# Kernel optimization log

Hardware: AMD Instinct MI355X
Metric: run time of the kernel (lower is better)

## Reference

```python
import jax, jax.numpy as jnp
import numpy as np

R = 32            # voxel resolution
DIM = 240         # channels C
EPS_NORM = 0.0    # module eps
BN_EPS = 1e-5     # torch BatchNorm1d default eps


def setup_inputs() -> dict:
    key = jax.random.key(0)
    k1, k2, k3 = jax.random.split(key, 3)
    B, C, N = 4, DIM, 32768
    features = jax.random.normal(k1, (B, C, N), jnp.float32)
    coords = jax.random.uniform(k2, (B, 3, N), jnp.float32)
    # mlp params: Conv1d(2C -> C, kernel 1) + BatchNorm1d(C)
    w = jax.random.normal(k3, (C, 2 * C), jnp.float32) / np.sqrt(2 * C).astype(np.float32)
    b = jnp.zeros((C,), jnp.float32)
    gamma = jnp.ones((C,), jnp.float32)
    beta = jnp.zeros((C,), jnp.float32)
    return {"features": features, "coords": coords, "w": w, "b": b, "gamma": gamma, "beta": beta}


def _voxelize(features, coords):
    # normalize coords into [0, 1], scale to voxel grid
    nc = coords - coords.mean(axis=2, keepdims=True)                      # [B,3,N]
    scale = jnp.linalg.norm(nc, axis=1, keepdims=True).max(axis=2, keepdims=True) * 2.0 + EPS_NORM
    nc = nc / scale + 0.5
    nc = jnp.clip(nc * R, 0, R - 1)
    vox = jnp.round(nc).astype(jnp.int32)
    pos = vox[:, 0] + vox[:, 1] * R + vox[:, 2] * (R * R)                 # [B,N] flattened voxel id
    R3 = R * R * R

    def per_batch(f, p):
        # f: [C,N], p: [N] -> [2C, R3]; per-voxel max feature + second (min) feature
        mx = jax.ops.segment_max(f.T, p, num_segments=R3)                 # [R3, C]
        mn = jax.ops.segment_min(f.T, p, num_segments=R3)                 # [R3, C]
        cnt = jax.ops.segment_sum(jnp.ones_like(p), p, num_segments=R3)  # [R3]
        mask = (cnt > 0)[:, None]
        mx = jnp.where(mask, mx, 0.0)
        mn = jnp.where(mask, mn, 0.0)
        return jnp.concatenate([mx, mn], axis=1).T                        # [2C, R3]

    fea = jax.vmap(per_batch)(features, pos)                              # [B,2C,R3]
    return fea, nc


def reference(features, coords, w, b, gamma, beta):
    fea, nc = _voxelize(features, coords)
    # 1x1 Conv1d (pointwise GEMM) + BatchNorm1d (training-mode batch stats) + Swish
    y = jnp.einsum('co,bov->bcv', w, fea) + b[None, :, None]
    mean = y.mean(axis=(0, 2), keepdims=True)
    var = y.var(axis=(0, 2), keepdims=True)
    y = gamma[None, :, None] * (y - mean) * jax.lax.rsqrt(var + BN_EPS) + beta[None, :, None]
    y = y * jax.nn.sigmoid(y)
    B, C, _ = features.shape
    return y.reshape(B, C, R, R, R), nc
```

## Files before the change

kernel.cpp:

```cpp
#include <hip/hip_runtime.h>
#include <cstdint>
#include <cstddef>

#define RR 32
#define R3 32768
#define NPT 32768
#define CH 240
#define CH2 480
#define NB 4
#define Y_ELEMS 31457280

typedef __attribute__((ext_vector_type(8))) short short8v;
typedef __attribute__((ext_vector_type(4))) float float4v;

union u8pack { short8v v; unsigned short u[8]; };

static __device__ __forceinline__ float bf2f(unsigned short u) {
  return __uint_as_float(((unsigned int)u) << 16);
}
static __device__ __forceinline__ unsigned short f2bf(float f) {
  unsigned int u = __float_as_uint(f);
  u = (u + 0x7FFFu + ((u >> 16) & 1u)) >> 16;
  return (unsigned short)u;
}

static __device__ __forceinline__ void gl_lds16(const void* g, void* l) {
  __builtin_amdgcn_global_load_lds((const __attribute__((address_space(1))) unsigned int*)g,
                                   (__attribute__((address_space(3))) unsigned int*)l, 16, 0, 0);
}

__global__ void k_init(int* __restrict__ cnt, float* __restrict__ stats,
                       const float* __restrict__ w, unsigned short* __restrict__ wfrag) {
  int g = blockIdx.x * 256 + threadIdx.x;
  if (g < NB * R3) cnt[g] = 0;
  if (g < 1024) stats[g] = 0.0f;
  if (g < 14400) {
    int lane = g & 63, t = g >> 6;
    int mg = t / 75, r = t % 75;
    int kc = r / 5, mL = r % 5;
    int m = mg * 5 + mL;
    int ln = lane & 15, q = lane >> 4;
    const float* src = w + (size_t)(m * 16 + ln) * CH2 + kc * 32 + q * 8;
    u8pack pk;
#pragma unroll
    for (int j = 0; j < 8; j++) pk.u[j] = f2bf(src[j]);
    *(short8v*)&wfrag[(size_t)g * 8] = pk.v;
  }
}

__global__ __launch_bounds__(1024) void k_coord_stats(const float* __restrict__ coords,
                                                      float* __restrict__ ms) {
  __shared__ float red[1024];
  __shared__ float mean[3];
  int b = blockIdx.x, t = threadIdx.x;
  const float4* cb4 = (const float4*)(coords + (size_t)b * 3 * NPT);
  float s[3] = {0.f, 0.f, 0.f};
  for (int i = t; i < NPT / 4; i += 1024) {
#pragma unroll
    for (int d = 0; d < 3; d++) {
      float4 v = cb4[d * (NPT / 4) + i];
      s[d] += (v.x + v.y) + (v.z + v.w);
    }
  }
  for (int d = 0; d < 3; d++) {
    red[t] = s[d]; __syncthreads();
    for (int k = 512; k > 0; k >>= 1) { if (t < k) red[t] += red[t + k]; __syncthreads(); }
    if (t == 0) mean[d] = red[0] * (1.0f / NPT);
    __syncthreads();
  }
  float m0 = mean[0], m1 = mean[1], m2 = mean[2];
  float mx = 0.f;
  for (int i = t; i < NPT / 4; i += 1024) {
    float4 x = cb4[i], y = cb4[NPT / 4 + i], z = cb4[2 * (NPT / 4) + i];
    float dx, dy, dz, n;
    dx = x.x - m0; dy = y.x - m1; dz = z.x - m2; n = dx * dx + dy * dy + dz * dz; mx = fmaxf(mx, n);
    dx = x.y - m0; dy = y.y - m1; dz = z.y - m2; n = dx * dx + dy * dy + dz * dz; mx = fmaxf(mx, n);
    dx = x.z - m0; dy = y.z - m1; dz = z.z - m2; n = dx * dx + dy * dy + dz * dz; mx = fmaxf(mx, n);
    dx = x.w - m0; dy = y.w - m1; dz = z.w - m2; n = dx * dx + dy * dy + dz * dz; mx = fmaxf(mx, n);
  }
  red[t] = mx; __syncthreads();
  for (int k = 512; k > 0; k >>= 1) { if (t < k) red[t] = fmaxf(red[t], red[t + k]); __syncthreads(); }
  if (t == 0) {
    ms[b * 4 + 0] = m0; ms[b * 4 + 1] = m1; ms[b * 4 + 2] = m2;
    ms[b * 4 + 3] = sqrtf(red[0]) * 2.0f;
  }
}

__global__ void k_pos_nc(const float* __restrict__ coords, const float* __restrict__ ms,
                         float* __restrict__ ncout, int* __restrict__ pos, int* __restrict__ cnt) {
  int g = blockIdx.x * 256 + threadIdx.x;
  int b = g >> 15, i = g & (NPT - 1);
  const float* cb = coords + (size_t)b * 3 * NPT;
  float scale = ms[b * 4 + 3];
  int vox[3];
#pragma unroll
  for (int d = 0; d < 3; d++) {
    float v = (cb[(size_t)d * NPT + i] - ms[b * 4 + d]) / scale + 0.5f;
    v = fminf(fmaxf(v * (float)RR, 0.0f), (float)(RR - 1));
    ncout[((size_t)(b * 3 + d)) * NPT + i] = v;
    vox[d] = (int)rintf(v);
  }
  int p = (b << 15) | (vox[0] + (vox[1] << 5) + (vox[2] << 10));
  pos[g] = p;
  atomicAdd(&cnt[p], 1);
}

__global__ void k_scan(const int* __restrict__ cnt, int* __restrict__ offs) {
  __shared__ int part[1024];
  int b = blockIdx.x, t = threadIdx.x;
  const int base = b * R3;
  int local[32];
  int s = 0;
#pragma unroll
  for (int j = 0; j < 32; j++) { local[j] = cnt[base + t * 32 + j]; s += local[j]; }
  part[t] = s; __syncthreads();
  for (int d = 1; d < 1024; d <<= 1) {
    int v = (t >= d) ? part[t - d] : 0;
    __syncthreads();
    part[t] += v;
    __syncthreads();
  }
  int run = (t == 0) ? 0 : part[t - 1];
#pragma unroll
  for (int j = 0; j < 32; j++) { offs[base + t * 32 + j] = run; run += local[j]; }
}

__global__ void k_scatter(const int* __restrict__ pos, int* __restrict__ offs,
                          int* __restrict__ sorted) {
  int g = blockIdx.x * 256 + threadIdx.x;
  int p = pos[g];
  int slot = atomicAdd(&offs[p], 1);
  sorted[((g >> 15) << 15) + slot] = g;
}

__global__ void k_transpose3(const float* __restrict__ f, unsigned short* __restrict__ ft) {
  __shared__ float tile[CH * 65];
  int p0 = blockIdx.x * 64, b = blockIdx.y;
  int t = threadIdx.x;
  {
    int pp = t & 63, cq = t >> 6;
    const float* src = f + ((size_t)b * CH) * NPT + p0 + pp;
#pragma unroll 4
    for (int j = 0; j < 60; ++j) {
      int c = j * 4 + cq;
      tile[c * 65 + pp] = src[(size_t)c * NPT];
    }
  }
  __syncthreads();
  int ch8 = t & 7;
#pragma unroll
  for (int pass = 0; pass < 2; ++pass) {
    int p = pass * 32 + (t >> 3);
    unsigned short* dst = ft + ((size_t)(b * NPT + p0 + p)) * CH;
#pragma unroll
    for (int i = 0; i < 4; ++i) {
      int ch = ch8 + 8 * i;
      if (ch < 30) {
        u8pack pk;
#pragma unroll
        for (int jj = 0; jj < 8; ++jj) pk.u[jj] = f2bf(tile[(ch * 8 + jj) * 65 + p]);
        *(short8v*)&dst[ch * 8] = pk.v;
      }
    }
  }
}

__global__ __launch_bounds__(256) void k_voxel4(const int* __restrict__ cnt,
                                                const int* __restrict__ offs,
                                                const int* __restrict__ sorted,
                                                const unsigned short* __restrict__ ft,
                                                unsigned short* __restrict__ feaf) {
  __shared__ unsigned short sh[7680];
  int bcg = blockIdx.x;
  int b = bcg >> 11;
  int wave = threadIdx.x >> 6, lane = threadIdx.x & 63;
  int sub = lane >> 5, l = lane & 31;
  int vbase = bcg << 4;
#pragma unroll
  for (int it = 0; it < 2; ++it) {
    int ln = wave + 8 * it + 4 * sub;
    if (l < 30) {
      int v = vbase + ln;
      int t0 = l, t1 = 30 + l;
      int idx0 = (t0 >> 2) * 512 + ((t0 & 3) * 16 + ln) * 8;
      int idx1 = (t1 >> 2) * 512 + ((t1 & 3) * 16 + ln) * 8;
      int n = cnt[v];
      if (n == 0) {
        u8pack z;
#pragma unroll
        for (int j = 0; j < 8; j++) z.u[j] = 0;
        *(short8v*)&sh[idx0] = z.v;
        *(short8v*)&sh[idx1] = z.v;
      } else {
        int start = offs[v] - n;
        const int* sp = sorted + (b << 15) + start;
        float mx[8], mn[8];
#pragma unroll
        for (int j = 0; j < 8; j++) { mx[j] = -__builtin_inff(); mn[j] = __builtin_inff(); }
        int j = 0;
        for (; j + 2 <= n; j += 2) {
          int r0 = sp[j], r1 = sp[j + 1];
          u8pack u0, u1;
          u0.v = *(const short8v*)(ft + (size_t)r0 * CH + l * 8);
          u1.v = *(const short8v*)(ft + (size_t)r1 * CH + l * 8);
#pragma unroll
          for (int k = 0; k < 8; k++) {
            float a = bf2f(u0.u[k]), c = bf2f(u1.u[k]);
            mx[k] = fmaxf(mx[k], fmaxf(a, c));
            mn[k] = fminf(mn[k], fminf(a, c));
          }
        }
        if (j < n) {
          int r0 = sp[j];
          u8pack u0;
          u0.v = *(const short8v*)(ft + (size_t)r0 * CH + l * 8);
#pragma unroll
          for (int k = 0; k < 8; k++) {
            float a = bf2f(u0.u[k]);
            mx[k] = fmaxf(mx[k], a);
            mn[k] = fminf(mn[k], a);
          }
        }
        u8pack omx, omn;
#pragma unroll
        for (int k = 0; k < 8; k++) { omx.u[k] = f2bf(mx[k]); omn.u[k] = f2bf(mn[k]); }
        *(short8v*)&sh[idx0] = omx.v;
        *(short8v*)&sh[idx1] = omn.v;
      }
    }
  }
  __syncthreads();
  unsigned short* dst = feaf + (size_t)bcg * 7680;
  for (int i = threadIdx.x; i < 960; i += 256)
    *(int4*)&dst[i * 8] = *(const int4*)&sh[i * 8];
}

__global__ __launch_bounds__(256, 2) void k_gemm6(const unsigned short* __restrict__ wfrag,
                                                  const unsigned short* __restrict__ feaf,
                                                  const float* __restrict__ bias,
                                                  unsigned short* __restrict__ ybf,
                                                  float* __restrict__ gstats) {
  __shared__ unsigned short wl[75 * 512];
  __shared__ float bstats[160];
  int wave = threadIdx.x >> 6, lane = threadIdx.x & 63;
  int ln = lane & 15, q = lane >> 4;
  int mg = blockIdx.y, bz = blockIdx.z;

  for (int i = threadIdx.x; i < 160; i += 256) bstats[i] = 0.0f;

  {
    const unsigned short* gs = wfrag + (size_t)mg * 75 * 512 + lane * 8;
    for (int i = wave; i < 75; i += 4) gl_lds16(gs + i * 512, wl + i * 512);
  }

  int v0 = blockIdx.x * 256 + wave * 64;
  int cg0 = v0 >> 4;
  const unsigned short* fbb = feaf + ((size_t)(bz * 2048 + cg0) * 15) * 512 + lane * 8;

  float4v acc[5][4];
#pragma unroll
  for (int m = 0; m < 5; m++)
#pragma unroll
    for (int j = 0; j < 4; j++) acc[m][j] = (float4v){0.f, 0.f, 0.f, 0.f};

  short8v cb0 = *(const short8v*)(fbb + (size_t)(0 * 15 + 0) * 512);
  short8v cb1 = *(const short8v*)(fbb + (size_t)(1 * 15 + 0) * 512);
  short8v cb2 = *(const short8v*)(fbb + (size_t)(2 * 15 + 0) * 512);
  short8v cb3 = *(const short8v*)(fbb + (size_t)(3 * 15 + 0) * 512);

  __syncthreads();

#pragma unroll
  for (int kc = 0; kc < 15; ++kc) {
    short8v nb0, nb1, nb2, nb3;
    if (kc < 14) {
      nb0 = *(const short8v*)(fbb + (size_t)(0 * 15 + kc + 1) * 512);
      nb1 = *(const short8v*)(fbb + (size_t)(1 * 15 + kc + 1) * 512);
      nb2 = *(const short8v*)(fbb + (size_t)(2 * 15 + kc + 1) * 512);
      nb3 = *(const short8v*)(fbb + (size_t)(3 * 15 + kc + 1) * 512);
    }
    const unsigned short* wp = wl + (size_t)(kc * 5) * 512 + lane * 8;
#pragma unroll
    for (int mL = 0; mL < 5; ++mL) {
      short8v a = *(const short8v*)(wp + (size_t)mL * 512);
      acc[mL][0] = __builtin_amdgcn_mfma_f32_16x16x32_bf16(a, cb0, acc[mL][0], 0, 0, 0);
      acc[mL][1] = __builtin_amdgcn_mfma_f32_16x16x32_bf16(a, cb1, acc[mL][1], 0, 0, 0);
      acc[mL][2] = __builtin_amdgcn_mfma_f32_16x16x32_bf16(a, cb2, acc[mL][2], 0, 0, 0);
      acc[mL][3] = __builtin_amdgcn_mfma_f32_16x16x32_bf16(a, cb3, acc[mL][3], 0, 0, 0);
    }
    if (kc < 14) { cb0 = nb0; cb1 = nb1; cb2 = nb2; cb3 = nb3; }
  }

  unsigned short* yb = ybf + ((size_t)bz * CH) * R3 + v0 + ln;
#pragma unroll
  for (int mL = 0; mL < 5; ++mL) {
#pragma unroll
    for (int r = 0; r < 4; ++r) {
      int cl = mL * 16 + q * 4 + r;
      int c = mg * 80 + cl;
      float bb = bias[c];
      float y0 = acc[mL][0][r] + bb;
      float y1 = acc[mL][1][r] + bb;
      float y2 = acc[mL][2][r] + bb;
      float y3 = acc[mL][3][r] + bb;
      unsigned short* yrow = yb + (size_t)c * R3;
      yrow[0] = f2bf(y0); yrow[16] = f2bf(y1); yrow[32] = f2bf(y2); yrow[48] = f2bf(y3);
      float s = (y0 + y1) + (y2 + y3);
      float sq = (y0 * y0 + y1 * y1) + (y2 * y2 + y3 * y3);
#pragma unroll
      for (int off = 1; off < 16; off <<= 1) {
        s += __shfl_xor(s, off);
        sq += __shfl_xor(sq, off);
      }
      if (ln == 0) {
        atomicAdd(&bstats[cl], s);
        atomicAdd(&bstats[80 + cl], sq);
      }
    }
  }
  __syncthreads();
  for (int i = threadIdx.x; i < 160; i += 256) {
    int g = (i < 80) ? (mg * 80 + i) : (CH + mg * 80 + (i - 80));
    atomicAdd(&gstats[g], bstats[i]);
  }
}

__global__ void k_apply(const unsigned short* __restrict__ ybf, float* __restrict__ out,
                        const float* __restrict__ stats, const float* __restrict__ gamma,
                        const float* __restrict__ beta) {
  int g = blockIdx.x * 256 + threadIdx.x;
  int c = (g >> 12) % CH;
  const float ninv = 1.0f / (float)(NB * R3);
  float mean = stats[c] * ninv;
  float var = stats[CH + c] * ninv - mean * mean;
  float s = gamma[c] * rsqrtf(var + 1e-5f);
  float h = beta[c] - mean * s;
  u8pack v;
  v.v = *(const short8v*)(ybf + (size_t)g * 8);
  float4 o0, o1;
  float t;
  t = bf2f(v.u[0]) * s + h; o0.x = t / (1.0f + __expf(-t));
  t = bf2f(v.u[1]) * s + h; o0.y = t / (1.0f + __expf(-t));
  t = bf2f(v.u[2]) * s + h; o0.z = t / (1.0f + __expf(-t));
  t = bf2f(v.u[3]) * s + h; o0.w = t / (1.0f + __expf(-t));
  t = bf2f(v.u[4]) * s + h; o1.x = t / (1.0f + __expf(-t));
  t = bf2f(v.u[5]) * s + h; o1.y = t / (1.0f + __expf(-t));
  t = bf2f(v.u[6]) * s + h; o1.z = t / (1.0f + __expf(-t));
  t = bf2f(v.u[7]) * s + h; o1.w = t / (1.0f + __expf(-t));
  ((float4*)out)[(size_t)g * 2] = o0;
  ((float4*)out)[(size_t)g * 2 + 1] = o1;
}

extern "C" void kernel_launch(void* const* d_in, const int* in_sizes, int n_in,
                              void* d_out, int out_size, void* d_ws, size_t ws_size,
                              hipStream_t stream) {
  const float* features = (const float*)d_in[0];
  const float* coords   = (const float*)d_in[1];
  const float* w        = (const float*)d_in[2];
  const float* bias     = (const float*)d_in[3];
  const float* gamma    = (const float*)d_in[4];
  const float* beta     = (const float*)d_in[5];
  float* out = (float*)d_out;

  char* ws = (char*)d_ws;
  size_t off = 0;
  float* ms    = (float*)(ws + off); off += 256;
  float* stats = (float*)(ws + off); off += 4096;
  int* pos     = (int*)(ws + off);   off += (size_t)NB * NPT * 4;
  int* cnt     = (int*)(ws + off);   off += (size_t)NB * R3 * 4;
  int* offs    = (int*)(ws + off);   off += (size_t)NB * R3 * 4;
  int* sorted  = (int*)(ws + off);   off += (size_t)NB * NPT * 4;
  unsigned short* wfrag = (unsigned short*)(ws + off); off += (size_t)CH * CH2 * 2;
  unsigned short* ft    = (unsigned short*)(ws + off); off += (size_t)NB * NPT * CH * 2;
  unsigned short* feaf  = (unsigned short*)(ws + off); off += (size_t)NB * R3 * CH2 * 2;
  unsigned short* ybf   = ft;

  float* ncout = out + Y_ELEMS;

  k_init<<<516, 256, 0, stream>>>(cnt, stats, w, wfrag);
  k_coord_stats<<<4, 1024, 0, stream>>>(coords, ms);
  k_pos_nc<<<512, 256, 0, stream>>>(coords, ms, ncout, pos, cnt);
  k_scan<<<4, 1024, 0, stream>>>(cnt, offs);
  k_scatter<<<512, 256, 0, stream>>>(pos, offs, sorted);
  k_transpose3<<<dim3(512, 4), 256, 0, stream>>>(features, ft);
  k_voxel4<<<NB * 2048, 256, 0, stream>>>(cnt, offs, sorted, ft, feaf);
  k_gemm6<<<dim3(128, 3, NB), 256, 0, stream>>>(wfrag, feaf, bias, ybf, stats);
  k_apply<<<Y_ELEMS / 2048, 256, 0, stream>>>(ybf, out, stats, gamma, beta);
}
```

Before: 399.0 us.

## Fuse voxel reduction into GEMM and write transposed features in sorted order

The transpose kernel now scatters each point's bf16 feature row straight to its voxel-sorted slot, using a per-point rank from the scatter kernel. The voxel max/min gather therefore reads contiguous rows and no longer chases indices. The voxel reduction is fused with the 1x1-conv GEMM in one 512-thread kernel: pooled features stay in swizzled LDS, and each wave keeps its weight fragments in registers across all 240 output channels. This drops the feaf intermediate round-trip through global memory and a kernel launch. The cost is higher register and LDS pressure, plus scattered writes in the transpose.

```diff
diff --git a/kernel.cpp b/kernel.cpp
--- a/kernel.cpp
+++ b/kernel.cpp
@@ -22,11 +22,6 @@
   unsigned int u = __float_as_uint(f);
   u = (u + 0x7FFFu + ((u >> 16) & 1u)) >> 16;
   return (unsigned short)u;
-}
-
-static __device__ __forceinline__ void gl_lds16(const void* g, void* l) {
-  __builtin_amdgcn_global_load_lds((const __attribute__((address_space(1))) unsigned int*)g,
-                                   (__attribute__((address_space(3))) unsigned int*)l, 16, 0, 0);
 }
 
 __global__ void k_init(int* __restrict__ cnt, float* __restrict__ stats,
@@ -126,17 +121,20 @@
 }
 
 __global__ void k_scatter(const int* __restrict__ pos, int* __restrict__ offs,
-                          int* __restrict__ sorted) {
+                          int* __restrict__ rank) {
   int g = blockIdx.x * 256 + threadIdx.x;
   int p = pos[g];
   int slot = atomicAdd(&offs[p], 1);
-  sorted[((g >> 15) << 15) + slot] = g;
-}
-
-__global__ void k_transpose3(const float* __restrict__ f, unsigned short* __restrict__ ft) {
+  rank[g] = slot;
+}
+
+__global__ void k_transpose3(const float* __restrict__ f, const int* __restrict__ rank,
+                             unsigned short* __restrict__ fts) {
   __shared__ float tile[CH * 65];
+  __shared__ int slts[64];
   int p0 = blockIdx.x * 64, b = blockIdx.y;
   int t = threadIdx.x;
+  if (t < 64) slts[t] = rank[b * NPT + p0 + t];
   {
     int pp = t & 63, cq = t >> 6;
     const float* src = f + ((size_t)b * CH) * NPT + p0 + pp;
@@ -151,7 +149,7 @@
 #pragma unroll
   for (int pass = 0; pass < 2; ++pass) {
     int p = pass * 32 + (t >> 3);
-    unsigned short* dst = ft + ((size_t)(b * NPT + p0 + p)) * CH;
+    unsigned short* dst = fts + ((size_t)(b * NPT + slts[p])) * CH;
 #pragma unroll
     for (int i = 0; i < 4; ++i) {
       int ch = ch8 + 8 * i;
@@ -165,55 +163,70 @@
   }
 }
 
-__global__ __launch_bounds__(256) void k_voxel4(const int* __restrict__ cnt,
-                                                const int* __restrict__ offs,
-                                                const int* __restrict__ sorted,
-                                                const unsigned short* __restrict__ ft,
-                                                unsigned short* __restrict__ feaf) {
-  __shared__ unsigned short sh[7680];
-  int bcg = blockIdx.x;
-  int b = bcg >> 11;
-  int wave = threadIdx.x >> 6, lane = threadIdx.x & 63;
+__global__ __launch_bounds__(512, 2) void k_fused(const int* __restrict__ cnt,
+                                                  const int* __restrict__ offs,
+                                                  const unsigned short* __restrict__ fts,
+                                                  const unsigned short* __restrict__ wfrag,
+                                                  const float* __restrict__ bias,
+                                                  unsigned short* __restrict__ ybf,
+                                                  float* __restrict__ gstats) {
+  __shared__ unsigned short fB[8 * 15 * 512];
+  __shared__ float bstats[480];
+  int tid = threadIdx.x;
+  int wave = tid >> 6, lane = tid & 63;
   int sub = lane >> 5, l = lane & 31;
-  int vbase = bcg << 4;
-#pragma unroll
-  for (int it = 0; it < 2; ++it) {
-    int ln = wave + 8 * it + 4 * sub;
+  int ln = lane & 15, q = lane >> 4;
+  int b = blockIdx.y;
+  int v0 = blockIdx.x * 128;
+  int bbase = b << 15;
+
+  for (int i = tid; i < 480; i += 512) bstats[i] = 0.0f;
+
+  int proc = wave * 2 + sub;
+  int t1c = 30 + l;
+  int kc0 = l >> 2, q0 = l & 3;
+  int kc1 = t1c >> 2, q1 = t1c & 3;
+#pragma unroll 1
+  for (int it = 0; it < 8; ++it) {
     if (l < 30) {
-      int v = vbase + ln;
-      int t0 = l, t1 = 30 + l;
-      int idx0 = (t0 >> 2) * 512 + ((t0 & 3) * 16 + ln) * 8;
-      int idx1 = (t1 >> 2) * 512 + ((t1 & 3) * 16 + ln) * 8;
+      int v = bbase + v0 + it * 16 + proc;
+      int ci0 = (q0 * 16 + proc) ^ ((kc0 & 3) << 1);
+      int ci1 = (q1 * 16 + proc) ^ ((kc1 & 3) << 1);
+      int idx0 = ((it * 15 + kc0) * 64 + ci0) * 8;
+      int idx1 = ((it * 15 + kc1) * 64 + ci1) * 8;
       int n = cnt[v];
       if (n == 0) {
         u8pack z;
 #pragma unroll
-        for (int j = 0; j < 8; j++) z.u[j] = 0;
-        *(short8v*)&sh[idx0] = z.v;
-        *(short8v*)&sh[idx1] = z.v;
+        for (int k = 0; k < 8; k++) z.u[k] = 0;
+        *(short8v*)&fB[idx0] = z.v;
+        *(short8v*)&fB[idx1] = z.v;
       } else {
         int start = offs[v] - n;
-        const int* sp = sorted + (b << 15) + start;
+        const unsigned short* sp = fts + (size_t)(bbase + start) * CH + l * 8;
         float mx[8], mn[8];
 #pragma unroll
-        for (int j = 0; j < 8; j++) { mx[j] = -__builtin_inff(); mn[j] = __builtin_inff(); }
+        for (int k = 0; k < 8; k++) { mx[k] = -__builtin_inff(); mn[k] = __builtin_inff(); }
         int j = 0;
-        for (; j + 2 <= n; j += 2) {
-          int r0 = sp[j], r1 = sp[j + 1];
-          u8pack u0, u1;
-          u0.v = *(const short8v*)(ft + (size_t)r0 * CH + l * 8);
-          u1.v = *(const short8v*)(ft + (size_t)r1 * CH + l * 8);
+        for (; j + 4 <= n; j += 4) {
+          u8pack u0, u1, u2, u3;
+          u0.v = *(const short8v*)(sp);
+          u1.v = *(const short8v*)(sp + CH);
+          u2.v = *(const short8v*)(sp + 2 * CH);
+          u3.v = *(const short8v*)(sp + 3 * CH);
+          sp += 4 * CH;
 #pragma unroll
           for (int k = 0; k < 8; k++) {
-            float a = bf2f(u0.u[k]), c = bf2f(u1.u[k]);
-            mx[k] = fmaxf(mx[k], fmaxf(a, c));
-            mn[k] = fminf(mn[k], fminf(a, c));
+            float a0 = bf2f(u0.u[k]), a1 = bf2f(u1.u[k]);
+            float a2 = bf2f(u2.u[k]), a3 = bf2f(u3.u[k]);
+            mx[k] = fmaxf(mx[k], fmaxf(fmaxf(a0, a1), fmaxf(a2, a3)));
+            mn[k] = fminf(mn[k], fminf(fminf(a0, a1), fminf(a2, a3)));
           }
         }
-        if (j < n) {
-          int r0 = sp[j];
+        for (; j < n; ++j) {
           u8pack u0;
-          u0.v = *(const short8v*)(ft + (size_t)r0 * CH + l * 8);
+          u0.v = *(const short8v*)(sp);
+          sp += CH;
 #pragma unroll
           for (int k = 0; k < 8; k++) {
             float a = bf2f(u0.u[k]);
@@ -224,103 +237,79 @@
         u8pack omx, omn;
 #pragma unroll
         for (int k = 0; k < 8; k++) { omx.u[k] = f2bf(mx[k]); omn.u[k] = f2bf(mn[k]); }
-        *(short8v*)&sh[idx0] = omx.v;
-        *(short8v*)&sh[idx1] = omn.v;
+        *(short8v*)&fB[idx0] = omx.v;
+        *(short8v*)&fB[idx1] = omn.v;
       }
     }
   }
+
+  int nmt = (wave == 7) ? 1 : 2;
+  short8v wreg[2][15];
+#pragma unroll
+  for (int mm = 0; mm < 2; ++mm)
+    if (mm < nmt) {
+      int mt = wave * 2 + mm;
+      int mg = mt / 5, mL = mt % 5;
+      const unsigned short* wp = wfrag + ((size_t)(mg * 75 + mL) * 512) + lane * 8;
+#pragma unroll
+      for (int kc = 0; kc < 15; ++kc)
+        wreg[mm][kc] = *(const short8v*)(wp + (size_t)kc * 5 * 512);
+    }
+
   __syncthreads();
-  unsigned short* dst = feaf + (size_t)bcg * 7680;
-  for (int i = threadIdx.x; i < 960; i += 256)
-    *(int4*)&dst[i * 8] = *(const int4*)&sh[i * 8];
-}
-
-__global__ __launch_bounds__(256, 2) void k_gemm6(const unsigned short* __restrict__ wfrag,
-                                                  const unsigned short* __restrict__ feaf,
-                                                  const float* __restrict__ bias,
-                                                  unsigned short* __restrict__ ybf,
-                                                  float* __restrict__ gstats) {
-  __shared__ unsigned short wl[75 * 512];
-  __shared__ float bstats[160];
-  int wave = threadIdx.x >> 6, lane = threadIdx.x & 63;
-  int ln = lane & 15, q = lane >> 4;
-  int mg = blockIdx.y, bz = blockIdx.z;
-
-  for (int i = threadIdx.x; i < 160; i += 256) bstats[i] = 0.0f;
-
-  {
-    const unsigned short* gs = wfrag + (size_t)mg * 75 * 512 + lane * 8;
-    for (int i = wave; i < 75; i += 4) gl_lds16(gs + i * 512, wl + i * 512);
-  }
-
-  int v0 = blockIdx.x * 256 + wave * 64;
-  int cg0 = v0 >> 4;
-  const unsigned short* fbb = feaf + ((size_t)(bz * 2048 + cg0) * 15) * 512 + lane * 8;
-
-  float4v acc[5][4];
-#pragma unroll
-  for (int m = 0; m < 5; m++)
-#pragma unroll
-    for (int j = 0; j < 4; j++) acc[m][j] = (float4v){0.f, 0.f, 0.f, 0.f};
-
-  short8v cb0 = *(const short8v*)(fbb + (size_t)(0 * 15 + 0) * 512);
-  short8v cb1 = *(const short8v*)(fbb + (size_t)(1 * 15 + 0) * 512);
-  short8v cb2 = *(const short8v*)(fbb + (size_t)(2 * 15 + 0) * 512);
-  short8v cb3 = *(const short8v*)(fbb + (size_t)(3 * 15 + 0) * 512);
-
+
+  float4v acc[2][8];
+#pragma unroll
+  for (int mm = 0; mm < 2; ++mm)
+#pragma unroll
+    for (int cg = 0; cg < 8; ++cg) acc[mm][cg] = (float4v){0.f, 0.f, 0.f, 0.f};
+
+#pragma unroll
+  for (int kc = 0; kc < 15; ++kc) {
+    const unsigned short* fbl = fB + (size_t)((lane ^ ((kc & 3) << 1)) * 8);
+    short8v bf[8];
+#pragma unroll
+    for (int cg = 0; cg < 8; ++cg)
+      bf[cg] = *(const short8v*)(fbl + (size_t)(cg * 15 + kc) * 512);
+#pragma unroll
+    for (int mm = 0; mm < 2; ++mm)
+      if (mm < nmt)
+#pragma unroll
+        for (int cg = 0; cg < 8; ++cg)
+          acc[mm][cg] = __builtin_amdgcn_mfma_f32_16x16x32_bf16(wreg[mm][kc], bf[cg], acc[mm][cg], 0, 0, 0);
+  }
+
+  unsigned short* yb = ybf + ((size_t)b * CH) * R3 + v0 + ln;
+#pragma unroll
+  for (int mm = 0; mm < 2; ++mm)
+    if (mm < nmt) {
+      int mt = wave * 2 + mm;
+#pragma unroll
+      for (int r = 0; r < 4; ++r) {
+        int c = mt * 16 + q * 4 + r;
+        float bb = bias[c];
+        unsigned short* yrow = yb + (size_t)c * R3;
+        float s = 0.f, sq = 0.f;
+#pragma unroll
+        for (int cg = 0; cg < 8; ++cg) {
+          float yv = acc[mm][cg][r] + bb;
+          yrow[cg * 16] = f2bf(yv);
+          s += yv; sq += yv * yv;
+        }
+#pragma unroll
+        for (int off = 1; off < 16; off <<= 1) {
+          s += __shfl_xor(s, off);
+          sq += __shfl_xor(sq, off);
+        }
+        if (ln == 0) {
+          atomicAdd(&bstats[c], s);
+          atomicAdd(&bstats[240 + c], sq);
+        }
+      }
+    }
   __syncthreads();
-
-#pragma unroll
-  for (int kc = 0; kc < 15; ++kc) {
-    short8v nb0, nb1, nb2, nb3;
-    if (kc < 14) {
-      nb0 = *(const short8v*)(fbb + (size_t)(0 * 15 + kc + 1) * 512);
-      nb1 = *(const short8v*)(fbb + (size_t)(1 * 15 + kc + 1) * 512);
-      nb2 = *(const short8v*)(fbb + (size_t)(2 * 15 + kc + 1) * 512);
-      nb3 = *(const short8v*)(fbb + (size_t)(3 * 15 + kc + 1) * 512);
-    }
-    const unsigned short* wp = wl + (size_t)(kc * 5) * 512 + lane * 8;
-#pragma unroll
-    for (int mL = 0; mL < 5; ++mL) {
-      short8v a = *(const short8v*)(wp + (size_t)mL * 512);
-      acc[mL][0] = __builtin_amdgcn_mfma_f32_16x16x32_bf16(a, cb0, acc[mL][0], 0, 0, 0);
-      acc[mL][1] = __builtin_amdgcn_mfma_f32_16x16x32_bf16(a, cb1, acc[mL][1], 0, 0, 0);
-      acc[mL][2] = __builtin_amdgcn_mfma_f32_16x16x32_bf16(a, cb2, acc[mL][2], 0, 0, 0);
-      acc[mL][3] = __builtin_amdgcn_mfma_f32_16x16x32_bf16(a, cb3, acc[mL][3], 0, 0, 0);
-    }
-    if (kc < 14) { cb0 = nb0; cb1 = nb1; cb2 = nb2; cb3 = nb3; }
-  }
-
-  unsigned short* yb = ybf + ((size_t)bz * CH) * R3 + v0 + ln;
-#pragma unroll
-  for (int mL = 0; mL < 5; ++mL) {
-#pragma unroll
-    for (int r = 0; r < 4; ++r) {
-      int cl = mL * 16 + q * 4 + r;
-      int c = mg * 80 + cl;
-      float bb = bias[c];
-      float y0 = acc[mL][0][r] + bb;
-      float y1 = acc[mL][1][r] + bb;
-      float y2 = acc[mL][2][r] + bb;
-      float y3 = acc[mL][3][r] + bb;
-      unsigned short* yrow = yb + (size_t)c * R3;
-      yrow[0] = f2bf(y0); yrow[16] = f2bf(y1); yrow[32] = f2bf(y2); yrow[48] = f2bf(y3);
-      float s = (y0 + y1) + (y2 + y3);
-      float sq = (y0 * y0 + y1 * y1) + (y2 * y2 + y3 * y3);
-#pragma unroll
-      for (int off = 1; off < 16; off <<= 1) {
-        s += __shfl_xor(s, off);
-        sq += __shfl_xor(sq, off);
-      }
-      if (ln == 0) {
-        atomicAdd(&bstats[cl], s);
-        atomicAdd(&bstats[80 + cl], sq);
-      }
-    }
-  }
-  __syncthreads();
-  for (int i = threadIdx.x; i < 160; i += 256) {
-    int g = (i < 80) ? (mg * 80 + i) : (CH + mg * 80 + (i - 80));
+  for (int i = tid; i < 480; i += 512) {
+    int g = (i < 240) ? i : (CH + (i - 240));
     atomicAdd(&gstats[g], bstats[i]);
   }
 }
@@ -369,11 +358,10 @@
   int* pos     = (int*)(ws + off);   off += (size_t)NB * NPT * 4;
   int* cnt     = (int*)(ws + off);   off += (size_t)NB * R3 * 4;
   int* offs    = (int*)(ws + off);   off += (size_t)NB * R3 * 4;
-  int* sorted  = (int*)(ws + off);   off += (size_t)NB * NPT * 4;
+  int* rank    = (int*)(ws + off);   off += (size_t)NB * NPT * 4;
   unsigned short* wfrag = (unsigned short*)(ws + off); off += (size_t)CH * CH2 * 2;
-  unsigned short* ft    = (unsigned short*)(ws + off); off += (size_t)NB * NPT * CH * 2;
-  unsigned short* feaf  = (unsigned short*)(ws + off); off += (size_t)NB * R3 * CH2 * 2;
-  unsigned short* ybf   = ft;
+  unsigned short* fts   = (unsigned short*)(ws + off); off += (size_t)NB * NPT * CH * 2;
+  unsigned short* ybf   = (unsigned short*)(ws + off); off += (size_t)NB * R3 * CH * 2;
 
   float* ncout = out + Y_ELEMS;
 
@@ -381,9 +369,8 @@
   k_coord_stats<<<4, 1024, 0, stream>>>(coords, ms);
   k_pos_nc<<<512, 256, 0, stream>>>(coords, ms, ncout, pos, cnt);
   k_scan<<<4, 1024, 0, stream>>>(cnt, offs);
-  k_scatter<<<512, 256, 0, stream>>>(pos, offs, sorted);
-  k_transpose3<<<dim3(512, 4), 256, 0, stream>>>(features, ft);
-  k_voxel4<<<NB * 2048, 256, 0, stream>>>(cnt, offs, sorted, ft, feaf);
-  k_gemm6<<<dim3(128, 3, NB), 256, 0, stream>>>(wfrag, feaf, bias, ybf, stats);
+  k_scatter<<<512, 256, 0, stream>>>(pos, offs, rank);
+  k_transpose3<<<dim3(512, 4), 256, 0, stream>>>(features, rank, fts);
+  k_fused<<<dim3(256, NB), 512, 0, stream>>>(cnt, offs, fts, wfrag, bias, ybf, stats);
   k_apply<<<Y_ELEMS / 2048, 256, 0, stream>>>(ybf, out, stats, gamma, beta);
 }
```

After: 394.8 us. Within noise of the previous version (-1.1%).
